# Kernel optimization log

Hardware: AMD Instinct MI355X
Metric: run time of the kernel (lower is better)

## Reference

```python
import jax, jax.numpy as jnp
import numpy as np

N = 8192  # input_size
DT = 1.0
TAU1, TAU2, TAU3 = 20.0, 50.0, 100.0


def _corr(a, b):
    # Pearson correlation of two equal-length vectors (torch.corrcoef[0,1]), NaN -> 0
    ac = a - jnp.mean(a)
    bc = b - jnp.mean(b)
    c = jnp.sum(ac * bc) / jnp.sqrt(jnp.sum(ac * ac) * jnp.sum(bc * bc))
    return jnp.where(jnp.isnan(c), jnp.zeros_like(c), c)


def setup_inputs() -> dict:
    key = jax.random.key(0)
    ks = jax.random.split(key, 8)
    return {
        'sensory_motor_input': jax.random.normal(ks[0], (N,), jnp.float32),
        'layer1_state': jax.random.normal(ks[1], (N,), jnp.float32),
        'layer2_state': jax.random.normal(ks[2], (N // 2,), jnp.float32),
        'layer3_state': jax.random.normal(ks[3], (N // 4,), jnp.float32),
        'w12': jax.random.normal(ks[4], (N // 2, N), jnp.float32) * 0.1,
        'w23': jax.random.normal(ks[5], (N // 4, N // 2), jnp.float32) * 0.1,
        'w32': jax.random.normal(ks[6], (N // 2, N // 4), jnp.float32) * 0.1,
        'w21': jax.random.normal(ks[7], (N, N // 2), jnp.float32) * 0.1,
        'correlation_strength': jnp.zeros((), jnp.float32),
        'neural_coherence': jnp.zeros((), jnp.float32),
    }


def reference(sensory_motor_input, layer1_state, layer2_state, layer3_state,
              w12, w23, w32, w21, correlation_strength, neural_coherence):
    # Layer 1: direct sensorimotor, exponential decay toward tanh target
    l1_target = jnp.tanh(sensory_motor_input)
    d1 = 1.0 - DT / TAU1
    l1 = d1 * layer1_state + (1.0 - d1) * l1_target

    # Layer 2: bottom-up + 0.3 * top-down feedback
    l2_in = w12 @ l1 + 0.3 * (w32 @ layer3_state)
    d2 = 1.0 - DT / TAU2
    l2 = d2 * layer2_state + (1.0 - d2) * jnp.tanh(l2_in)

    # Layer 3: meta feedback
    d3 = 1.0 - DT / TAU3
    l3 = d3 * layer3_state + (1.0 - d3) * jnp.tanh(w23 @ l2)

    # Cross-layer correlations (truncate the larger vector)
    c12 = _corr(l1[: l2.shape[0]], l2)
    c23 = _corr(l2[: l3.shape[0]], l3)
    corr_new = 0.9 * correlation_strength + 0.1 * (c12 + c23) / 2.0

    total_activity = jnp.sum(jnp.abs(l1)) + jnp.sum(jnp.abs(l2)) + jnp.sum(jnp.abs(l3))
    activity_variance = jnp.var(jnp.concatenate([l1, l2, l3]), ddof=1)  # torch.var unbiased
    coherence = total_activity / (activity_variance + 1e-6)
    coh_new = 0.9 * neural_coherence + 0.1 * jnp.clip(coherence, 0.0, 10.0)

    hier_activity = total_activity / (N + N // 2 + N // 4)
    return (l1, l2, l3, corr_new, coh_new, hier_activity)
```

## Files before the change

kernel.cpp:

```cpp
#include <hip/hip_runtime.h>
#include <math.h>

#define N1 8192
#define N2 4096
#define N3 2048

typedef float f4 __attribute__((ext_vector_type(4)));

__device__ __forceinline__ float dot4(f4 u, f4 x, float acc) {
    return fmaf(u.x, x.x, fmaf(u.y, x.y, fmaf(u.z, x.z, fmaf(u.w, x.w, acc))));
}

__global__ __launch_bounds__(256) void kA(const float* __restrict__ smi,
                                          const float* __restrict__ l1s,
                                          const float* __restrict__ w12,
                                          const float* __restrict__ w32,
                                          const float* __restrict__ w23,
                                          const float* __restrict__ l3s,
                                          const float* __restrict__ l2s,
                                          float* __restrict__ a_out,
                                          float* __restrict__ b_out,
                                          float* __restrict__ A_out,
                                          float* __restrict__ l1_out) {
    __shared__ float lds[N1];
    const int blk = blockIdx.x;
    const int t = threadIdx.x;

    if (blk < 1024) {
        __shared__ float ws[4][4];
        const int r0 = blk * 4;
        {
            const f4* __restrict__ s4 = reinterpret_cast<const f4*>(smi);
            const f4* __restrict__ p4 = reinterpret_cast<const f4*>(l1s);
            f4* __restrict__ d4 = reinterpret_cast<f4*>(lds);
#pragma unroll
            for (int k = 0; k < 8; ++k) {
                const int i = t + k * 256;
                f4 s = s4[i];
                f4 p = p4[i];
                f4 r;
                r.x = fmaf(0.95f, p.x, 0.05f * tanhf(s.x));
                r.y = fmaf(0.95f, p.y, 0.05f * tanhf(s.y));
                r.z = fmaf(0.95f, p.z, 0.05f * tanhf(s.z));
                r.w = fmaf(0.95f, p.w, 0.05f * tanhf(s.w));
                d4[i] = r;
            }
        }
        __syncthreads();
        if (blk < 32) {
            const int i = blk * 256 + t;
            l1_out[i] = lds[i];
        }
        const f4* __restrict__ w0 = reinterpret_cast<const f4*>(w12) + (size_t)r0 * (N1 / 4);
        const f4* __restrict__ w1 = w0 + (N1 / 4);
        const f4* __restrict__ w2 = w1 + (N1 / 4);
        const f4* __restrict__ w3 = w2 + (N1 / 4);
        const f4* __restrict__ x1 = reinterpret_cast<const f4*>(lds);
        float a0 = 0.f, a1 = 0.f, a2 = 0.f, a3 = 0.f;
#pragma unroll
        for (int k = 0; k < 8; ++k) {
            const int i = t + k * 256;
            f4 xv = x1[i];
            a0 = dot4(__builtin_nontemporal_load(&w0[i]), xv, a0);
            a1 = dot4(__builtin_nontemporal_load(&w1[i]), xv, a1);
            a2 = dot4(__builtin_nontemporal_load(&w2[i]), xv, a2);
            a3 = dot4(__builtin_nontemporal_load(&w3[i]), xv, a3);
        }
#pragma unroll
        for (int off = 32; off; off >>= 1) {
            a0 += __shfl_down(a0, off, 64);
            a1 += __shfl_down(a1, off, 64);
            a2 += __shfl_down(a2, off, 64);
            a3 += __shfl_down(a3, off, 64);
        }
        if ((t & 63) == 0) {
            const int w = t >> 6;
            ws[w][0] = a0; ws[w][1] = a1; ws[w][2] = a2; ws[w][3] = a3;
        }
        __syncthreads();
        if (t < 4) a_out[r0 + t] = ws[0][t] + ws[1][t] + ws[2][t] + ws[3][t];
    } else if (blk < 1280) {
        __shared__ float ws[4][16];
        const int r0 = (blk - 1024) * 16;
        const f4* __restrict__ base = reinterpret_cast<const f4*>(w32) + (size_t)r0 * (N3 / 4);
        const f4* __restrict__ x3 = reinterpret_cast<const f4*>(l3s);
        f4 x0 = x3[t];
        f4 x1v = x3[t + 256];
        float acc[16];
#pragma unroll
        for (int rr = 0; rr < 16; ++rr) {
            f4 u0 = __builtin_nontemporal_load(&base[(size_t)rr * (N3 / 4) + t]);
            f4 u1 = __builtin_nontemporal_load(&base[(size_t)rr * (N3 / 4) + 256 + t]);
            acc[rr] = dot4(u1, x1v, dot4(u0, x0, 0.f));
        }
#pragma unroll
        for (int rr = 0; rr < 16; ++rr) {
            float v = acc[rr];
#pragma unroll
            for (int off = 32; off; off >>= 1) v += __shfl_down(v, off, 64);
            acc[rr] = v;
        }
        if ((t & 63) == 0) {
            const int w = t >> 6;
#pragma unroll
            for (int rr = 0; rr < 16; ++rr) ws[w][rr] = acc[rr];
        }
        __syncthreads();
        if (t < 16) b_out[r0 + t] = ws[0][t] + ws[1][t] + ws[2][t] + ws[3][t];
    } else {
        __shared__ float ws[4][8];
        const int r0 = (blk - 1280) * 8;
        const f4* __restrict__ base = reinterpret_cast<const f4*>(w23) + (size_t)r0 * (N2 / 4);
        const f4* __restrict__ xs = reinterpret_cast<const f4*>(l2s);
        f4 xv[4];
#pragma unroll
        for (int k = 0; k < 4; ++k) xv[k] = xs[t + k * 256];
        float acc[8];
#pragma unroll
        for (int rr = 0; rr < 8; ++rr) {
            float v = 0.f;
#pragma unroll
            for (int k = 0; k < 4; ++k)
                v = dot4(__builtin_nontemporal_load(&base[(size_t)rr * (N2 / 4) + k * 256 + t]), xv[k], v);
            acc[rr] = v;
        }
#pragma unroll
        for (int rr = 0; rr < 8; ++rr) {
            float v = acc[rr];
#pragma unroll
            for (int off = 32; off; off >>= 1) v += __shfl_down(v, off, 64);
            acc[rr] = v;
        }
        if ((t & 63) == 0) {
            const int w = t >> 6;
#pragma unroll
            for (int rr = 0; rr < 8; ++rr) ws[w][rr] = acc[rr];
        }
        __syncthreads();
        if (t < 8) A_out[r0 + t] = ws[0][t] + ws[1][t] + ws[2][t] + ws[3][t];
    }
}

__global__ __launch_bounds__(256) void kB(const float* __restrict__ w23,
                                          const float* __restrict__ a_in,
                                          const float* __restrict__ b_in,
                                          const float* __restrict__ A_in,
                                          const float* __restrict__ l2s,
                                          const float* __restrict__ l3s,
                                          float* __restrict__ l2_out,
                                          float* __restrict__ l3_out) {
    __shared__ float lds_l2[N2];
    __shared__ float ws[4][8];
    const int t = threadIdx.x;
    const int blk = blockIdx.x;

    {
        const f4* __restrict__ a4 = reinterpret_cast<const f4*>(a_in);
        const f4* __restrict__ b4 = reinterpret_cast<const f4*>(b_in);
        const f4* __restrict__ s4 = reinterpret_cast<const f4*>(l2s);
        f4* __restrict__ d4 = reinterpret_cast<f4*>(lds_l2);
#pragma unroll
        for (int k = 0; k < 4; ++k) {
            const int i = t + k * 256;
            f4 av = a4[i];
            f4 bv = b4[i];
            f4 sv = s4[i];
            f4 r;
            r.x = fmaf(0.98f, sv.x, 0.02f * tanhf(fmaf(0.3f, bv.x, av.x)));
            r.y = fmaf(0.98f, sv.y, 0.02f * tanhf(fmaf(0.3f, bv.y, av.y)));
            r.z = fmaf(0.98f, sv.z, 0.02f * tanhf(fmaf(0.3f, bv.z, av.z)));
            r.w = fmaf(0.98f, sv.w, 0.02f * tanhf(fmaf(0.3f, bv.w, av.w)));
            d4[i] = r;
        }
    }
    __syncthreads();
    if (blk < 16) {
        const int i = blk * 256 + t;
        l2_out[i] = lds_l2[i];
    }

    const int r0 = blk * 8;
    const f4* __restrict__ base = reinterpret_cast<const f4*>(w23) + (size_t)r0 * (N2 / 4);
    const f4* __restrict__ xl = reinterpret_cast<const f4*>(lds_l2);
    f4 xv[4];
#pragma unroll
    for (int k = 0; k < 4; ++k) xv[k] = xl[t + k * 256];
    float acc[8];
#pragma unroll
    for (int rr = 0; rr < 8; ++rr) {
        float v = 0.f;
#pragma unroll
        for (int k = 0; k < 4; ++k)
            v = dot4(base[(size_t)rr * (N2 / 4) + k * 256 + t], xv[k], v);
        acc[rr] = v;
    }
#pragma unroll
    for (int rr = 0; rr < 8; ++rr) {
        float v = acc[rr];
#pragma unroll
        for (int off = 32; off; off >>= 1) v += __shfl_down(v, off, 64);
        acc[rr] = v;
    }
    if ((t & 63) == 0) {
        const int w = t >> 6;
#pragma unroll
        for (int rr = 0; rr < 8; ++rr) ws[w][rr] = acc[rr];
    }
    __syncthreads();
    if (t < 8) {
        const int r = r0 + t;
        float tot = ws[0][t] + ws[1][t] + ws[2][t] + ws[3][t];
        l3_out[r] = 0.99f * l3s[r] + 0.01f * tanhf(tot);
    }
    (void)A_in;
}

__global__ __launch_bounds__(1024) void k_fin(const float* __restrict__ out,
                                              const float* __restrict__ corr_in,
                                              const float* __restrict__ coh_in,
                                              float* __restrict__ scal) {
    __shared__ double sred[16][13];
    __shared__ double fin[13];
    const int t = threadIdx.x;
    const f4* __restrict__ o4 = reinterpret_cast<const f4*>(out);

    double p[13];
#pragma unroll
    for (int j = 0; j < 13; ++j) p[j] = 0.0;

    for (int i = t; i < 3584; i += 1024) {
        f4 v = o4[i];
#pragma unroll
        for (int c = 0; c < 4; ++c) {
            double d = (double)v[c];
            p[0] += fabs(d); p[1] += d; p[2] += d * d;
        }
    }
    {
        f4 x = o4[t];
        f4 y = o4[2048 + t];
#pragma unroll
        for (int c = 0; c < 4; ++c) {
            double dx = (double)x[c], dy = (double)y[c];
            p[3] += dx; p[4] += dy; p[5] += dx * dx; p[6] += dy * dy; p[7] += dx * dy;
        }
    }
    if (t < 512) {
        f4 x = o4[2048 + t];
        f4 y = o4[3072 + t];
#pragma unroll
        for (int c = 0; c < 4; ++c) {
            double dx = (double)x[c], dy = (double)y[c];
            p[8] += dx; p[9] += dy; p[10] += dx * dx; p[11] += dy * dy; p[12] += dx * dy;
        }
    }

#pragma unroll
    for (int j = 0; j < 13; ++j) {
        double v = p[j];
#pragma unroll
        for (int off = 32; off; off >>= 1) v += __shfl_down(v, off, 64);
        p[j] = v;
    }
    if ((t & 63) == 0) {
        const int w = t >> 6;
#pragma unroll
        for (int j = 0; j < 13; ++j) sred[w][j] = p[j];
    }
    __syncthreads();
    if (t < 13) {
        double s = 0.0;
#pragma unroll
        for (int w = 0; w < 16; ++w) s += sred[w][t];
        fin[t] = s;
    }
    __syncthreads();

    if (t == 0) {
        const double n12 = (double)N2;
        const double n23 = (double)N3;
        const double nall = (double)(N1 + N2 + N3);

        double sxy12 = fin[7] - fin[3] * fin[4] / n12;
        double sxx12 = fin[5] - fin[3] * fin[3] / n12;
        double syy12 = fin[6] - fin[4] * fin[4] / n12;
        double den12 = sqrt(sxx12 * syy12);
        double c12 = (den12 > 0.0 && isfinite(den12)) ? sxy12 / den12 : 0.0;

        double sxy23 = fin[12] - fin[8] * fin[9] / n23;
        double sxx23 = fin[10] - fin[8] * fin[8] / n23;
        double syy23 = fin[11] - fin[9] * fin[9] / n23;
        double den23 = sqrt(sxx23 * syy23);
        double c23 = (den23 > 0.0 && isfinite(den23)) ? sxy23 / den23 : 0.0;

        double corr_new = 0.9 * (double)corr_in[0] + 0.1 * (c12 + c23) * 0.5;

        double total = fin[0];
        double var = (fin[2] - fin[1] * fin[1] / nall) / (nall - 1.0);
        double coh = total / (var + 1e-6);
        coh = fmin(fmax(coh, 0.0), 10.0);
        double coh_new = 0.9 * (double)coh_in[0] + 0.1 * coh;

        scal[0] = (float)corr_new;
        scal[1] = (float)coh_new;
        scal[2] = (float)(total / nall);
    }
}

extern "C" void kernel_launch(void* const* d_in, const int* in_sizes, int n_in,
                              void* d_out, int out_size, void* d_ws, size_t ws_size,
                              hipStream_t stream) {
    const float* smi     = (const float*)d_in[0];
    const float* l1s     = (const float*)d_in[1];
    const float* l2s     = (const float*)d_in[2];
    const float* l3s     = (const float*)d_in[3];
    const float* w12     = (const float*)d_in[4];
    const float* w23     = (const float*)d_in[5];
    const float* w32     = (const float*)d_in[6];
    const float* corr_in = (const float*)d_in[8];
    const float* coh_in  = (const float*)d_in[9];

    float* out = (float*)d_out;
    float* l1 = out;
    float* l2 = out + N1;
    float* l3 = out + N1 + N2;
    float* scal = out + N1 + N2 + N3;

    float* a_ws = (float*)d_ws;
    float* b_ws = a_ws + N2;
    float* A_ws = b_ws + N2;

    kA<<<dim3(1536), dim3(256), 0, stream>>>(smi, l1s, w12, w32, w23, l3s, l2s,
                                             a_ws, b_ws, A_ws, l1);
    kB<<<dim3(256), dim3(256), 0, stream>>>(w23, a_ws, b_ws, A_ws, l2s, l3s, l2, l3);
    k_fin<<<dim3(1), dim3(1024), 0, stream>>>(out, corr_in, coh_in, scal);
}
```

Baseline: 58.72 us.

## Cache w23 in kA for reuse in kB and double kB grid parallelism

kA's pass over w23 (which computes an unused A_out) now uses normal loads instead of nontemporal loads, so w23 can stay in L2/LLC for kB's real w23 GEMV. kB now handles 4 rows per block over 512 blocks instead of 8 rows over 256, spreading the memory-bound GEMV across more CUs. The unused A_in parameter is dropped. Normal loads could evict other data, and the extra blocks each redo the l2 tanh preamble.

```diff
diff --git a/kernel.cpp b/kernel.cpp
--- a/kernel.cpp
+++ b/kernel.cpp
@@ -121,7 +121,7 @@
             float v = 0.f;
 #pragma unroll
             for (int k = 0; k < 4; ++k)
-                v = dot4(__builtin_nontemporal_load(&base[(size_t)rr * (N2 / 4) + k * 256 + t]), xv[k], v);
+                v = dot4(base[(size_t)rr * (N2 / 4) + k * 256 + t], xv[k], v);
             acc[rr] = v;
         }
 #pragma unroll
@@ -144,13 +144,12 @@
 __global__ __launch_bounds__(256) void kB(const float* __restrict__ w23,
                                           const float* __restrict__ a_in,
                                           const float* __restrict__ b_in,
-                                          const float* __restrict__ A_in,
                                           const float* __restrict__ l2s,
                                           const float* __restrict__ l3s,
                                           float* __restrict__ l2_out,
                                           float* __restrict__ l3_out) {
     __shared__ float lds_l2[N2];
-    __shared__ float ws[4][8];
+    __shared__ float ws[4][4];
     const int t = threadIdx.x;
     const int blk = blockIdx.x;
 
@@ -179,40 +178,39 @@
         l2_out[i] = lds_l2[i];
     }
 
-    const int r0 = blk * 8;
-    const f4* __restrict__ base = reinterpret_cast<const f4*>(w23) + (size_t)r0 * (N2 / 4);
+    const int r0 = blk * 4;
+    const f4* __restrict__ w0 = reinterpret_cast<const f4*>(w23) + (size_t)r0 * (N2 / 4);
+    const f4* __restrict__ w1 = w0 + (N2 / 4);
+    const f4* __restrict__ w2 = w1 + (N2 / 4);
+    const f4* __restrict__ w3 = w2 + (N2 / 4);
     const f4* __restrict__ xl = reinterpret_cast<const f4*>(lds_l2);
-    f4 xv[4];
-#pragma unroll
-    for (int k = 0; k < 4; ++k) xv[k] = xl[t + k * 256];
-    float acc[8];
-#pragma unroll
-    for (int rr = 0; rr < 8; ++rr) {
-        float v = 0.f;
-#pragma unroll
-        for (int k = 0; k < 4; ++k)
-            v = dot4(base[(size_t)rr * (N2 / 4) + k * 256 + t], xv[k], v);
-        acc[rr] = v;
-    }
-#pragma unroll
-    for (int rr = 0; rr < 8; ++rr) {
-        float v = acc[rr];
-#pragma unroll
-        for (int off = 32; off; off >>= 1) v += __shfl_down(v, off, 64);
-        acc[rr] = v;
+    float a0 = 0.f, a1 = 0.f, a2 = 0.f, a3 = 0.f;
+#pragma unroll
+    for (int k = 0; k < 4; ++k) {
+        const int i = t + k * 256;
+        f4 xv = xl[i];
+        a0 = dot4(w0[i], xv, a0);
+        a1 = dot4(w1[i], xv, a1);
+        a2 = dot4(w2[i], xv, a2);
+        a3 = dot4(w3[i], xv, a3);
+    }
+#pragma unroll
+    for (int off = 32; off; off >>= 1) {
+        a0 += __shfl_down(a0, off, 64);
+        a1 += __shfl_down(a1, off, 64);
+        a2 += __shfl_down(a2, off, 64);
+        a3 += __shfl_down(a3, off, 64);
     }
     if ((t & 63) == 0) {
         const int w = t >> 6;
-#pragma unroll
-        for (int rr = 0; rr < 8; ++rr) ws[w][rr] = acc[rr];
+        ws[w][0] = a0; ws[w][1] = a1; ws[w][2] = a2; ws[w][3] = a3;
     }
     __syncthreads();
-    if (t < 8) {
+    if (t < 4) {
         const int r = r0 + t;
         float tot = ws[0][t] + ws[1][t] + ws[2][t] + ws[3][t];
         l3_out[r] = 0.99f * l3s[r] + 0.01f * tanhf(tot);
     }
-    (void)A_in;
 }
 
 __global__ __launch_bounds__(1024) void k_fin(const float* __restrict__ out,
@@ -332,6 +330,6 @@
 
     kA<<<dim3(1536), dim3(256), 0, stream>>>(smi, l1s, w12, w32, w23, l3s, l2s,
                                              a_ws, b_ws, A_ws, l1);
-    kB<<<dim3(256), dim3(256), 0, stream>>>(w23, a_ws, b_ws, A_ws, l2s, l3s, l2, l3);
+    kB<<<dim3(512), dim3(256), 0, stream>>>(w23, a_ws, b_ws, l2s, l3s, l2, l3);
     k_fin<<<dim3(1), dim3(1024), 0, stream>>>(out, corr_in, coh_in, scal);
 }
```

Result: slower. 60.45 us (+2.9%).
